# Optimization experiments

Measured on AMD Instinct MI355X. Metric: run time of the kernel, lower is better.

The kernel has to match this reference:

```python
import jax, jax.numpy as jnp
import numpy as np

D_MODEL, N_QUERY, N_HEAD = 1024, 2, 8
D_HEAD = D_MODEL // (N_QUERY * N_HEAD)  # 64
KV = D_HEAD * N_HEAD                    # 512


def setup_inputs() -> dict:
    key = jax.random.key(0)
    ks = jax.random.split(key, 6)
    B, S = 2, 2048
    x = jax.random.normal(ks[0], (B, S, D_MODEL), jnp.float32)
    Wq = jax.random.normal(ks[1], (D_MODEL, D_MODEL), jnp.float32) / np.sqrt(D_MODEL)
    Wk = jax.random.normal(ks[2], (D_MODEL, KV), jnp.float32) / np.sqrt(D_MODEL)
    Wv = jax.random.normal(ks[3], (D_MODEL, KV), jnp.float32) / np.sqrt(D_MODEL)
    memory = jax.random.normal(ks[4], (KV, KV), jnp.float32)
    memory_norm = jnp.ones((KV,), jnp.float32)
    memory_weight = jnp.ones((1,), jnp.float32)
    return {"x": x, "Wq": Wq, "Wk": Wk, "Wv": Wv,
            "memory": memory, "memory_norm": memory_norm,
            "memory_weight": memory_weight}


def reference(x, Wq, Wk, Wv, memory, memory_norm, memory_weight):
    B, S, _ = x.shape
    QH = N_QUERY * N_HEAD
    scale = 1.0 / jnp.sqrt(jnp.float32(D_HEAD))

    q = x @ Wq          # (B,S,D_MODEL)
    k = x @ Wk          # (B,S,KV)
    v = x @ Wv          # (B,S,KV)

    # --- Eq. 6: grouped scaled dot-product attention ---
    q4 = q.reshape(B, S, QH, D_HEAD)                    # flat query split
    k4 = jnp.repeat(k.reshape(B, S, N_HEAD, D_HEAD), N_QUERY, axis=2)  # (B,S,QH,D)
    v4 = jnp.repeat(v.reshape(B, S, N_HEAD, D_HEAD), N_QUERY, axis=2)
    scores = jnp.einsum('bsnd,btnd->bnst', q4, k4) * scale  # (B,QH,S,S)
    probs = jax.nn.softmax(scores, axis=-1)
    a_dot = jnp.einsum('bnst,btnd->bsnd', probs, v4)        # (B,S,QH,D)

    # --- Eq. 7: memory read (grouped over n_query, width n_head*d_head) ---
    sigma_q = jax.nn.elu(q.reshape(B, S, N_QUERY, KV))      # (B,S,Q,KV)
    num = sigma_q @ memory                                   # (B,S,Q,KV)
    den = (sigma_q @ memory_norm)[..., None]                 # (B,S,Q,1)
    a_mem = (num / den).reshape(B, S, QH, D_HEAD)

    # --- Eq. 8/9: memory update (delta rule) ---
    sigma_k = jax.nn.elu(k)                                  # (B,S,KV)
    retrieved = (sigma_k @ memory) / (sigma_k @ memory_norm)[..., None]
    new_memory = memory + jnp.einsum('bsk,bsv->kv', sigma_k, v - retrieved)
    new_memory_norm = memory_norm + jnp.sum(sigma_k, axis=(0, 1))

    # --- Eq. 10: sigmoid-gated fusion ---
    w = jax.nn.sigmoid(memory_weight)                        # (1,)
    out = (a_dot * (1.0 - w) + a_mem * w).reshape(B, S, D_MODEL)
    return out, new_memory, new_memory_norm
```

## Files before the change

### kernel.cpp

```cpp
#include <hip/hip_runtime.h>
#include <hip/hip_bf16.h>

#define BB 2
#define SS 2048
#define DM 1024
#define KVD 512
#define NH 8
#define NQ 2
#define QH 16
#define DH 64
#define MROWS 4096

typedef float f32x4 __attribute__((ext_vector_type(4)));
typedef short short8 __attribute__((ext_vector_type(8)));
typedef short short4v __attribute__((ext_vector_type(4)));
typedef unsigned uint2v __attribute__((ext_vector_type(2)));

__device__ __forceinline__ float elu_f(float x) {
    return x > 0.0f ? x : (__expf(x) - 1.0f);
}

__device__ __forceinline__ short f2bf(float f) {
    union { float f; unsigned u; } v; v.f = f;
    unsigned r = v.u + 0x7FFFu + ((v.u >> 16) & 1u);
    return (short)(r >> 16);
}
__device__ __forceinline__ float bf2f(short s) {
    union { unsigned u; float f; } v;
    v.u = ((unsigned)(unsigned short)s) << 16;
    return v.f;
}
__device__ __forceinline__ unsigned cvtpk(float lo, float hi) {
    unsigned u;
    asm("v_cvt_pk_bf16_f32 %0, %1, %2" : "=v"(u) : "v"(lo), "v"(hi));
    return u;
}

__device__ __forceinline__ int swzs(int row, int byteoff) {
    return (row * 128 + (byteoff ^ ((row & 7) << 4))) >> 1;
}

#define GLD16(gp, lp) __builtin_amdgcn_global_load_lds( \
    (const __attribute__((address_space(1))) void*)(gp), \
    (__attribute__((address_space(3))) void*)(lp), 16, 0, 0)

__device__ __forceinline__ void stage_gl(const short* __restrict__ src, int ld,
                                         int row0, int k0, short* L,
                                         int wv, int lane) {
    const int srow = lane >> 3, sslot = lane & 7;
    #pragma unroll
    for (int i = 0; i < 4; i++) {
        int row = wv * 32 + i * 8 + srow;
        int slot = sslot ^ (row & 7);
        GLD16(&src[(size_t)(row0 + row) * ld + k0 + slot * 8],
              &L[(wv * 32 + i * 8) * 64]);
    }
}

__device__ __forceinline__ void stage_gl64(const short* __restrict__ src, int ld,
                                           int row0, int k0, short* L,
                                           int wv, int lane) {
    const int srow = lane >> 3, sslot = lane & 7;
    #pragma unroll
    for (int i = 0; i < 2; i++) {
        int row = wv * 16 + i * 8 + srow;
        int slot = sslot ^ (row & 7);
        GLD16(&src[(size_t)(row0 + row) * ld + k0 + slot * 8],
              &L[(wv * 16 + i * 8) * 64]);
    }
}

__device__ __forceinline__ void mma_tile(const short* __restrict__ Als,
                                         const short* __restrict__ Bls,
                                         int mb, int nb, int qr, int kg,
                                         f32x4 acc[4][4]) {
    #pragma unroll
    for (int kc = 0; kc < 2; kc++) {
        short8 af[4], bg[4];
        #pragma unroll
        for (int mi = 0; mi < 4; mi++)
            af[mi] = *(const short8*)&Als[swzs(mb + mi * 16 + qr, kc * 64 + kg * 16)];
        #pragma unroll
        for (int ni = 0; ni < 4; ni++)
            bg[ni] = *(const short8*)&Bls[swzs(nb + ni * 16 + qr, kc * 64 + kg * 16)];
        #pragma unroll
        for (int mi = 0; mi < 4; mi++)
            #pragma unroll
            for (int ni = 0; ni < 4; ni++)
                acc[mi][ni] = __builtin_amdgcn_mfma_f32_16x16x32_bf16(
                    af[mi], bg[ni], acc[mi][ni], 0, 0, 0);
    }
}

__device__ __forceinline__ void mma_tile64(const short* __restrict__ Als,
                                           const short* __restrict__ Bls,
                                           int mb, int nb, int qr, int kg,
                                           f32x4 acc[2][2]) {
    #pragma unroll
    for (int kc = 0; kc < 2; kc++) {
        short8 af[2], bg[2];
        #pragma unroll
        for (int mi = 0; mi < 2; mi++)
            af[mi] = *(const short8*)&Als[swzs(mb + mi * 16 + qr, kc * 64 + kg * 16)];
        #pragma unroll
        for (int ni = 0; ni < 2; ni++)
            bg[ni] = *(const short8*)&Bls[swzs(nb + ni * 16 + qr, kc * 64 + kg * 16)];
        #pragma unroll
        for (int mi = 0; mi < 2; mi++)
            #pragma unroll
            for (int ni = 0; ni < 2; ni++)
                acc[mi][ni] = __builtin_amdgcn_mfma_f32_16x16x32_bf16(
                    af[mi], bg[ni], acc[mi][ni], 0, 0, 0);
    }
}

__global__ __launch_bounds__(256) void prep_all(
        const float* __restrict__ x, const float* __restrict__ Wq,
        const float* __restrict__ Wk, const float* __restrict__ Wv,
        const float* __restrict__ memory,
        short* __restrict__ xb, short* __restrict__ wtb,
        short* __restrict__ memtb, float* __restrict__ out_mem) {
    __shared__ float Ts[64][65];
    const int blk = blockIdx.x;
    const int tid = threadIdx.x;

    if (blk < 2048) {
        int i = (blk * 256 + tid) * 8;
        float4 a = *(const float4*)&x[i];
        float4 b = *(const float4*)&x[i + 4];
        short8 s;
        s[0] = f2bf(a.x); s[1] = f2bf(a.y); s[2] = f2bf(a.z); s[3] = f2bf(a.w);
        s[4] = f2bf(b.x); s[5] = f2bf(b.y); s[6] = f2bf(b.z); s[7] = f2bf(b.w);
        *(short8*)&xb[i] = s;
        return;
    }
    if (blk < 2560) {
        int idx = blk - 2048;
        const int k0 = (idx & 15) * 64, n0 = (idx >> 4) * 64;
        const float* W; int ld, c0;
        if (n0 < 1024)      { W = Wq; ld = 1024; c0 = n0; }
        else if (n0 < 1536) { W = Wk; ld = 512;  c0 = n0 - 1024; }
        else                { W = Wv; ld = 512;  c0 = n0 - 1536; }
        #pragma unroll
        for (int i = 0; i < 16; i++) {
            int e = tid + 256 * i;
            int kk = e >> 6, nn = e & 63;
            Ts[nn][kk] = W[(size_t)(k0 + kk) * ld + c0 + nn];
        }
        __syncthreads();
        #pragma unroll
        for (int i = 0; i < 16; i++) {
            int e = tid + 256 * i;
            int nn = e >> 6, kk = e & 63;
            wtb[(size_t)(n0 + nn) * 1024 + k0 + kk] = f2bf(Ts[nn][kk]);
        }
        return;
    }
    if (blk < 2624) {
        int idx = blk - 2560;
        const int k0 = (idx & 7) * 64, n0 = (idx >> 3) * 64;
        #pragma unroll
        for (int i = 0; i < 16; i++) {
            int e = tid + 256 * i;
            int kk = e >> 6, nn = e & 63;
            Ts[nn][kk] = memory[(size_t)(k0 + kk) * 512 + n0 + nn];
        }
        __syncthreads();
        #pragma unroll
        for (int i = 0; i < 16; i++) {
            int e = tid + 256 * i;
            int nn = e >> 6, kk = e & 63;
            memtb[(size_t)(n0 + nn) * 512 + k0 + kk] = f2bf(Ts[nn][kk]);
        }
        return;
    }
    {
        int idx = blk - 2624;
        int i = (idx * 256 + tid) * 4;
        *(float4*)&out_mem[i] = *(const float4*)&memory[i];
    }
}

__global__ __launch_bounds__(256) void gemm_qkv_mfma(
        const short* __restrict__ xb, const short* __restrict__ wtb,
        short* __restrict__ q, short* __restrict__ k, short* __restrict__ v,
        short* __restrict__ qelu, short* __restrict__ kelu,
        short* __restrict__ keluT, short* __restrict__ vt) {
    __shared__ __align__(16) short SMEM[32768];
    short (*Tls)[130] = (short(*)[130])SMEM;
    const int n0 = blockIdx.x * 128, m0 = blockIdx.y * 128;
    const int tid = threadIdx.x, lane = tid & 63, wv = tid >> 6;
    const int qr = lane & 15, kg = lane >> 4;
    const int mb = (wv >> 1) * 64, nb = (wv & 1) * 64;

    f32x4 acc[4][4];
    #pragma unroll
    for (int i = 0; i < 4; i++)
        #pragma unroll
        for (int j = 0; j < 4; j++) acc[i][j] = (f32x4){0.f, 0.f, 0.f, 0.f};

    stage_gl(xb, 1024, m0, 0, SMEM, wv, lane);
    stage_gl(wtb, 1024, n0, 0, SMEM + 8192, wv, lane);

    for (int kt = 0; kt < 16; kt++) {
        const int cur = kt & 1;
        short* Acur = SMEM + cur * 16384;
        short* Bcur = Acur + 8192;
        __syncthreads();
        if (kt + 1 < 16) {
            short* Anxt = SMEM + (cur ^ 1) * 16384;
            stage_gl(xb, 1024, m0, (kt + 1) * 64, Anxt, wv, lane);
            stage_gl(wtb, 1024, n0, (kt + 1) * 64, Anxt + 8192, wv, lane);
        }
        mma_tile(Acur, Bcur, mb, nb, qr, kg, acc);
    }
    __syncthreads();

    const int kind = (n0 < 1024) ? 0 : (n0 < 1536) ? 1 : 2;
    #pragma unroll
    for (int mi = 0; mi < 4; mi++)
        #pragma unroll
        for (int ni = 0; ni < 4; ni++)
            #pragma unroll
            for (int r = 0; r < 4; r++) {
                int lr = mb + mi * 16 + kg * 4 + r;
                int lc = nb + ni * 16 + qr;
                int gr = m0 + lr;
                short val = f2bf(acc[mi][ni][r]);
                if (kind == 0) {
                    int gc = n0 + lc;
                    q[(size_t)gr * 1024 + gc] = val;
                    qelu[(size_t)gr * 1024 + gc] = f2bf(elu_f(bf2f(val)));
                } else if (kind == 1) {
                    int gc = (n0 - 1024) + lc;
                    k[(size_t)gr * 512 + gc] = val;
                    short ev = f2bf(elu_f(bf2f(val)));
                    kelu[(size_t)gr * 512 + gc] = ev;
                    Tls[lr][lc] = ev;
                } else {
                    int gc = (n0 - 1536) + lc;
                    v[(size_t)gr * 512 + gc] = val;
                    Tls[lr][lc] = val;
                }
            }

    if (kind == 0) return;
    __syncthreads();
    const int lane16 = tid & 15, rgrp = tid >> 4;
    #pragma unroll
    for (int p = 0; p < 8; p++) {
        int lc2 = p * 16 + rgrp;
        short8 s;
        #pragma unroll
        for (int e = 0; e < 8; e++) s[e] = Tls[lane16 * 8 + e][lc2];
        if (kind == 1) {
            int gcT = (n0 - 1024) + lc2;
            *(short8*)&keluT[(size_t)gcT * 4096 + m0 + lane16 * 8] = s;
        } else {
            int gc = (n0 - 1536) + lc2;
            int bh2 = (m0 >> 11) * 8 + (gc >> 6);
            *(short8*)&vt[((size_t)bh2 * 64 + (gc & 63)) * SS + (m0 & 2047)
                          + lane16 * 8] = s;
        }
    }
}

__global__ __launch_bounds__(256) void den_colsum(
        const short* __restrict__ qelu, const short* __restrict__ kelu,
        const short* __restrict__ keluT, const float* __restrict__ norm,
        float* __restrict__ den_q, float* __restrict__ den_k,
        float* __restrict__ out_norm) {
    const int wavei = threadIdx.x >> 6, lane = threadIdx.x & 63;
    const int blk = blockIdx.x;
    if (blk < 3072) {
        const int row = blk * 4 + wavei;
        const short* src; float* den;
        if (row < 8192) { src = qelu + (size_t)row * 512; den = den_q + row; }
        else { int rk = row - 8192; src = kelu + (size_t)rk * 512; den = den_k + rk; }
        short8 vv = *(const short8*)&src[lane * 8];
        float4 n0 = *(const float4*)&norm[lane * 8];
        float4 n1 = *(const float4*)&norm[lane * 8 + 4];
        float nn[8] = {n0.x, n0.y, n0.z, n0.w, n1.x, n1.y, n1.z, n1.w};
        float s = 0.0f;
        #pragma unroll
        for (int j = 0; j < 8; j++) s += bf2f(vv[j]) * nn[j];
        #pragma unroll
        for (int off = 32; off >= 1; off >>= 1) s += __shfl_xor(s, off);
        if (lane == 0) *den = s;
    } else {
        const int row = (blk - 3072) * 4 + wavei;
        float s = 0.0f;
        #pragma unroll
        for (int j = 0; j < 8; j++) {
            short8 vv = *(const short8*)&keluT[(size_t)row * 4096 + j * 512 + lane * 8];
            #pragma unroll
            for (int e = 0; e < 8; e++) s += bf2f(vv[e]);
        }
        #pragma unroll
        for (int off = 32; off >= 1; off >>= 1) s += __shfl_xor(s, off);
        if (lane == 0) out_norm[row] = norm[row] + s;
    }
}

__global__ __launch_bounds__(256) void gemm_amem_mfma(
        const short* __restrict__ qelu, const short* __restrict__ memtb,
        const short* __restrict__ adotb, const float* __restrict__ den_q,
        const float* __restrict__ mw, float* __restrict__ out) {
    __shared__ __align__(16) short SMEM[16384];
    const int n0 = blockIdx.x * 64, m0 = blockIdx.y * 64;
    const int tid = threadIdx.x, lane = tid & 63, wv = tid >> 6;
    const int qr = lane & 15, kg = lane >> 4;
    const int mb = (wv >> 1) * 32, nb = (wv & 1) * 32;
    const float wgt = 1.0f / (1.0f + __expf(-mw[0]));

    f32x4 acc[2][2];
    #pragma unroll
    for (int i = 0; i < 2; i++)
        #pragma unroll
        for (int j = 0; j < 2; j++) acc[i][j] = (f32x4){0.f, 0.f, 0.f, 0.f};

    stage_gl64(qelu, 512, m0, 0, SMEM, wv, lane);
    stage_gl64(memtb, 512, n0, 0, SMEM + 4096, wv, lane);
    for (int kt = 0; kt < 8; kt++) {
        const int cur = kt & 1;
        short* Acur = SMEM + cur * 8192;
        short* Bcur = Acur + 4096;
        __syncthreads();
        if (kt + 1 < 8) {
            short* Anxt = SMEM + (cur ^ 1) * 8192;
            stage_gl64(qelu, 512, m0, (kt + 1) * 64, Anxt, wv, lane);
            stage_gl64(memtb, 512, n0, (kt + 1) * 64, Anxt + 4096, wv, lane);
        }
        mma_tile64(Acur, Bcur, mb, nb, qr, kg, acc);
    }

    #pragma unroll
    for (int mi = 0; mi < 2; mi++) {
        int gr0 = m0 + mb + mi * 16 + kg * 4;
        float invd[4];
        #pragma unroll
        for (int r = 0; r < 4; r++) invd[r] = wgt / den_q[gr0 + r];
        #pragma unroll
        for (int ni = 0; ni < 2; ni++) {
            int gc = n0 + nb + ni * 16 + qr;
            #pragma unroll
            for (int r = 0; r < 4; r++) {
                size_t fo = (size_t)(gr0 + r) * 512 + gc;
                out[fo] = bf2f(adotb[fo]) * (1.0f - wgt)
                        + acc[mi][ni][r] * invd[r];
            }
        }
    }
}

__global__ __launch_bounds__(256) void gemm_u_mfma(
        const short* __restrict__ kelu, const short* __restrict__ memtb,
        const short* __restrict__ vb, const float* __restrict__ den_k,
        short* __restrict__ uT) {
    __shared__ __align__(16) short SMEM[16384];
    const int n0 = blockIdx.x * 64, m0 = blockIdx.y * 64;
    const int tid = threadIdx.x, lane = tid & 63, wv = tid >> 6;
    const int qr = lane & 15, kg = lane >> 4;
    const int mb = (wv >> 1) * 32, nb = (wv & 1) * 32;

    f32x4 acc[2][2];
    #pragma unroll
    for (int i = 0; i < 2; i++)
        #pragma unroll
        for (int j = 0; j < 2; j++) acc[i][j] = (f32x4){0.f, 0.f, 0.f, 0.f};

    stage_gl64(kelu, 512, m0, 0, SMEM, wv, lane);
    stage_gl64(memtb, 512, n0, 0, SMEM + 4096, wv, lane);
    for (int kt = 0; kt < 8; kt++) {
        const int cur = kt & 1;
        short* Acur = SMEM + cur * 8192;
        short* Bcur = Acur + 4096;
        __syncthreads();
        if (kt + 1 < 8) {
            short* Anxt = SMEM + (cur ^ 1) * 8192;
            stage_gl64(kelu, 512, m0, (kt + 1) * 64, Anxt, wv, lane);
            stage_gl64(memtb, 512, n0, (kt + 1) * 64, Anxt + 4096, wv, lane);
        }
        mma_tile64(Acur, Bcur, mb, nb, qr, kg, acc);
    }

    #pragma unroll
    for (int mi = 0; mi < 2; mi++) {
        int gr0 = m0 + mb + mi * 16 + kg * 4;
        float invd[4];
        #pragma unroll
        for (int r = 0; r < 4; r++) invd[r] = 1.0f / den_k[gr0 + r];
        #pragma unroll
        for (int ni = 0; ni < 2; ni++) {
            int gc = n0 + nb + ni * 16 + qr;
            short4v st;
            #pragma unroll
            for (int r = 0; r < 4; r++)
                st[r] = f2bf(bf2f(vb[(size_t)(gr0 + r) * 512 + gc])
                             - acc[mi][ni][r] * invd[r]);
            *(short4v*)&uT[(size_t)gc * 4096 + gr0] = st;
        }
    }
}

__global__ __launch_bounds__(256) void gemm_delta_mfma(
        const short* __restrict__ keluT, const short* __restrict__ uT,
        float* __restrict__ out_mem) {
    __shared__ __align__(16) short SMEM[16384];
    const int j0 = blockIdx.x * 64, i0 = blockIdx.y * 64;
    const int kcz = blockIdx.z;
    const int tid = threadIdx.x, lane = tid & 63, wv = tid >> 6;
    const int qr = lane & 15, kg = lane >> 4;
    const int mb = (wv >> 1) * 32, nb = (wv & 1) * 32;

    f32x4 acc[2][2];
    #pragma unroll
    for (int i = 0; i < 2; i++)
        #pragma unroll
        for (int j = 0; j < 2; j++) acc[i][j] = (f32x4){0.f, 0.f, 0.f, 0.f};

    stage_gl64(keluT, 4096, i0, kcz * 512, SMEM, wv, lane);
    stage_gl64(uT, 4096, j0, kcz * 512, SMEM + 4096, wv, lane);
    for (int kt = 0; kt < 8; kt++) {
        const int cur = kt & 1;
        short* Acur = SMEM + cur * 8192;
        short* Bcur = Acur + 4096;
        __syncthreads();
        if (kt + 1 < 8) {
            int k0 = kcz * 512 + (kt + 1) * 64;
            short* Anxt = SMEM + (cur ^ 1) * 8192;
            stage_gl64(keluT, 4096, i0, k0, Anxt, wv, lane);
            stage_gl64(uT, 4096, j0, k0, Anxt + 4096, wv, lane);
        }
        mma_tile64(Acur, Bcur, mb, nb, qr, kg, acc);
    }

    #pragma unroll
    for (int mi = 0; mi < 2; mi++)
        #pragma unroll
        for (int ni = 0; ni < 2; ni++)
            #pragma unroll
            for (int r = 0; r < 4; r++) {
                int gr = i0 + mb + mi * 16 + kg * 4 + r;
                int gc = j0 + nb + ni * 16 + qr;
                atomicAdd(&out_mem[(size_t)gr * 512 + gc], acc[mi][ni][r]);
            }
}

__global__ __launch_bounds__(256) void flash_attn_mfma(
        const short* __restrict__ qb, const short* __restrict__ kb,
        const short* __restrict__ vt, short* __restrict__ adotb) {
    __shared__ __align__(16) short Klds[2][4096];
    __shared__ __align__(16) short Vlds[2][4096];
    __shared__ __align__(16) short Plds[4096];

    const int id = blockIdx.x;
    const int low3 = id & 7, rest = id >> 3;
    const int xblk = rest & 31, bhhi = rest >> 5;
    const int bh = (bhhi << 3) | low3;
    const int r0 = xblk * 64;
    const int b = bh >> 4, qh = bh & 15;
    const int kvh = qh >> 1;
    const int tid = threadIdx.x;
    const int lane = tid & 63, wv = tid >> 6;
    const int qr = lane & 15, kg = lane >> 4;
    const float scale2 = 0.125f * 1.44269504f;

    const int srow = lane >> 3, sslot = lane & 7;

    const int krow0 = wv * 16 + srow, krow1 = krow0 + 8;
    const short* kp0 = kb + (size_t)(b * SS + krow0) * KVD + kvh * DH
                       + (sslot ^ (krow0 & 7)) * 8;
    const short* kp1 = kb + (size_t)(b * SS + krow1) * KVD + kvh * DH
                       + (sslot ^ (krow1 & 7)) * 8;
    const short* vp0 = vt + ((size_t)(b * NH + kvh) * DH + krow0) * SS
                       + (sslot ^ (krow0 & 7)) * 8;
    const short* vp1 = vt + ((size_t)(b * NH + kvh) * DH + krow1) * SS
                       + (sslot ^ (krow1 & 7)) * 8;

    short8 qa[2];
    {
        const short* qp = qb + (size_t)(b * SS + r0 + wv * 16 + qr) * DM + qh * DH;
        qa[0] = *(const short8*)&qp[kg * 8];
        qa[1] = *(const short8*)&qp[32 + kg * 8];
        #pragma unroll
        for (int e = 0; e < 8; e++) {
            qa[0][e] = f2bf(bf2f(qa[0][e]) * scale2);
            qa[1][e] = f2bf(bf2f(qa[1][e]) * scale2);
        }
    }
    short8 ones;
    #pragma unroll
    for (int e = 0; e < 8; e++) ones[e] = (short)0x3F80;

    f32x4 oacc[4];
    #pragma unroll
    for (int dt = 0; dt < 4; dt++) oacc[dt] = (f32x4){0.f, 0.f, 0.f, 0.f};
    f32x4 lacc = (f32x4){0.f, 0.f, 0.f, 0.f};

    short* Pw = Plds + wv * 1024;
    short* Kdst0 = &Klds[0][(wv * 16 + 0) * 64];
    short* Kdst1 = &Klds[0][(wv * 16 + 8) * 64];
    short* Vdst0 = &Vlds[0][(wv * 16 + 0) * 64];
    short* Vdst1 = &Vlds[0][(wv * 16 + 8) * 64];

    GLD16(kp0, Kdst0); GLD16(kp1, Kdst1);
    GLD16(vp0, Vdst0); GLD16(vp1, Vdst1);

    for (int it = 0; it < 32; ++it) {
        const int cur = it & 1;
        __syncthreads();
        if (it + 1 < 32) {
            kp0 += 64 * KVD; kp1 += 64 * KVD; vp0 += 64; vp1 += 64;
            int nb2 = (cur ^ 1) * 4096;
            GLD16(kp0, Kdst0 + nb2); GLD16(kp1, Kdst1 + nb2);
            GLD16(vp0, Vdst0 + nb2); GLD16(vp1, Vdst1 + nb2);
        }

        f32x4 sacc[4];
        #pragma unroll
        for (int j = 0; j < 4; j++) sacc[j] = (f32x4){0.f, 0.f, 0.f, 0.f};
        __builtin_amdgcn_s_setprio(1);
        #pragma unroll
        for (int c = 0; c < 2; c++) {
            #pragma unroll
            for (int j = 0; j < 4; j++) {
                short8 kf = *(const short8*)&Klds[cur][swzs(j * 16 + qr, kg * 16 + c * 64)];
                sacc[j] = __builtin_amdgcn_mfma_f32_16x16x32_bf16(kf, qa[c], sacc[j], 0, 0, 0);
            }
        }
        __builtin_amdgcn_s_setprio(0);

        #pragma unroll
        for (int j = 0; j < 4; j++) {
            float p0 = exp2f(sacc[j][0]);
            float p1 = exp2f(sacc[j][1]);
            float p2 = exp2f(sacc[j][2]);
            float p3 = exp2f(sacc[j][3]);
            uint2v u;
            u[0] = cvtpk(p0, p1);
            u[1] = cvtpk(p2, p3);
            *(uint2v*)&Pw[swzs(qr, j * 32 + kg * 8)] = u;
        }
        asm volatile("s_waitcnt lgkmcnt(0)" ::: "memory");
        __builtin_amdgcn_sched_barrier(0);

        __builtin_amdgcn_s_setprio(1);
        #pragma unroll
        for (int c = 0; c < 2; c++) {
            short8 pf = *(const short8*)&Pw[swzs(qr, kg * 16 + c * 64)];
            lacc = __builtin_amdgcn_mfma_f32_16x16x32_bf16(ones, pf, lacc, 0, 0, 0);
            #pragma unroll
            for (int dt = 0; dt < 4; dt++) {
                short8 vf = *(const short8*)&Vlds[cur][swzs(dt * 16 + qr, kg * 16 + c * 64)];
                oacc[dt] = __builtin_amdgcn_mfma_f32_16x16x32_bf16(vf, pf, oacc[dt], 0, 0, 0);
            }
        }
        __builtin_amdgcn_s_setprio(0);
    }

    float inv = 1.0f / lacc[0];
    short* ap = adotb + (size_t)(b * SS + r0 + wv * 16 + qr) * DM + qh * DH;
    #pragma unroll
    for (int dt = 0; dt < 4; dt++) {
        short4v st;
        #pragma unroll
        for (int r = 0; r < 4; r++) st[r] = f2bf(oacc[dt][r] * inv);
        *(short4v*)&ap[dt * 16 + kg * 4] = st;
    }
}

extern "C" void kernel_launch(void* const* d_in, const int* in_sizes, int n_in,
                              void* d_out, int out_size, void* d_ws, size_t ws_size,
                              hipStream_t stream) {
    const float* x      = (const float*)d_in[0];
    const float* Wq     = (const float*)d_in[1];
    const float* Wk     = (const float*)d_in[2];
    const float* Wv     = (const float*)d_in[3];
    const float* memory = (const float*)d_in[4];
    const float* mnorm  = (const float*)d_in[5];
    const float* mw     = (const float*)d_in[6];

    float* out_f   = (float*)d_out;
    float* out_mem = out_f + (size_t)MROWS * DM;
    float* out_nrm = out_mem + (size_t)KVD * KVD;

    short*  xb    = (short*)d_ws;
    short*  wtb   = xb + 4194304;
    short*  memtb = wtb + 2097152;
    short*  qb    = memtb + 262144;
    short*  kbuf  = qb + 4194304;
    short*  vbuf  = kbuf + 2097152;
    short*  vt    = vbuf + 2097152;
    short*  qelu  = vt + 2097152;
    short*  kelu  = qelu + 4194304;
    short*  keluT = kelu + 2097152;
    short*  uT    = keluT + 2097152;
    float*  den_q = (float*)(uT + 2097152);
    float*  den_k = den_q + 8192;
    short*  adotb = xb;

    prep_all<<<2880, 256, 0, stream>>>(x, Wq, Wk, Wv, memory, xb, wtb, memtb,
                                       out_mem);

    gemm_qkv_mfma<<<dim3(16, 32), 256, 0, stream>>>(xb, wtb, qb, kbuf, vbuf,
                                                    qelu, kelu, keluT, vt);

    flash_attn_mfma<<<1024, 256, 0, stream>>>(qb, kbuf, vt, adotb);

    den_colsum<<<3200, 256, 0, stream>>>(qelu, kelu, keluT, mnorm,
                                         den_q, den_k, out_nrm);

    gemm_amem_mfma<<<dim3(8, 128), 256, 0, stream>>>(qelu, memtb, adotb,
                                                     den_q, mw, out_f);

    gemm_u_mfma<<<dim3(8, 64), 256, 0, stream>>>(kelu, memtb, vbuf, den_k, uT);
    gemm_delta_mfma<<<dim3(8, 8, 8), 256, 0, stream>>>(keluT, uT, out_mem);
}
```

Baseline: 147.3 us.

## Split attention KV tile across wave pairs with 512-thread blocks and LDS reduction

Doubles the flash-attention block to 8 waves, pairing waves so each handles half of every 64-key tile for the same 16 query rows. Each wave computes half the scores, writes a smaller P tile, and accumulates partial O and row sums, which are combined through LDS at the end. The aim is more waves in flight to hide latency in the per-tile compute chain. In exchange it adds a final reduction with extra syncs, duplicates the Q loads, and shrinks the MFMA work per wave.

Result: slower. 152.8 us (+3.7%).

```diff
diff --git a/kernel.cpp b/kernel.cpp
--- a/kernel.cpp
+++ b/kernel.cpp
@@ -38,6 +38,9 @@
 
 __device__ __forceinline__ int swzs(int row, int byteoff) {
     return (row * 128 + (byteoff ^ ((row & 7) << 4))) >> 1;
+}
+__device__ __forceinline__ int swz32(int row, int byteoff) {
+    return (row * 64 + (byteoff ^ ((row & 3) << 4))) >> 1;
 }
 
 #define GLD16(gp, lp) __builtin_amdgcn_global_load_lds( \
@@ -447,7 +450,7 @@
             }
 }
 
-__global__ __launch_bounds__(256) void flash_attn_mfma(
+__global__ __launch_bounds__(512) void flash_attn_mfma(
         const short* __restrict__ qb, const short* __restrict__ kb,
         const short* __restrict__ vt, short* __restrict__ adotb) {
     __shared__ __align__(16) short Klds[2][4096];
@@ -463,24 +466,21 @@
     const int kvh = qh >> 1;
     const int tid = threadIdx.x;
     const int lane = tid & 63, wv = tid >> 6;
+    const int pair = wv >> 1, half = wv & 1;
     const int qr = lane & 15, kg = lane >> 4;
     const float scale2 = 0.125f * 1.44269504f;
 
     const int srow = lane >> 3, sslot = lane & 7;
 
-    const int krow0 = wv * 16 + srow, krow1 = krow0 + 8;
-    const short* kp0 = kb + (size_t)(b * SS + krow0) * KVD + kvh * DH
-                       + (sslot ^ (krow0 & 7)) * 8;
-    const short* kp1 = kb + (size_t)(b * SS + krow1) * KVD + kvh * DH
-                       + (sslot ^ (krow1 & 7)) * 8;
-    const short* vp0 = vt + ((size_t)(b * NH + kvh) * DH + krow0) * SS
-                       + (sslot ^ (krow0 & 7)) * 8;
-    const short* vp1 = vt + ((size_t)(b * NH + kvh) * DH + krow1) * SS
-                       + (sslot ^ (krow1 & 7)) * 8;
+    const int krow = wv * 8 + srow;
+    const short* kp = kb + (size_t)(b * SS + krow) * KVD + kvh * DH
+                      + (sslot ^ (krow & 7)) * 8;
+    const short* vp = vt + ((size_t)(b * NH + kvh) * DH + krow) * SS
+                      + (sslot ^ (krow & 7)) * 8;
 
     short8 qa[2];
     {
-        const short* qp = qb + (size_t)(b * SS + r0 + wv * 16 + qr) * DM + qh * DH;
+        const short* qp = qb + (size_t)(b * SS + r0 + pair * 16 + qr) * DM + qh * DH;
         qa[0] = *(const short8*)&qp[kg * 8];
         qa[1] = *(const short8*)&qp[32 + kg * 8];
         #pragma unroll
@@ -498,75 +498,89 @@
     for (int dt = 0; dt < 4; dt++) oacc[dt] = (f32x4){0.f, 0.f, 0.f, 0.f};
     f32x4 lacc = (f32x4){0.f, 0.f, 0.f, 0.f};
 
-    short* Pw = Plds + wv * 1024;
-    short* Kdst0 = &Klds[0][(wv * 16 + 0) * 64];
-    short* Kdst1 = &Klds[0][(wv * 16 + 8) * 64];
-    short* Vdst0 = &Vlds[0][(wv * 16 + 0) * 64];
-    short* Vdst1 = &Vlds[0][(wv * 16 + 8) * 64];
-
-    GLD16(kp0, Kdst0); GLD16(kp1, Kdst1);
-    GLD16(vp0, Vdst0); GLD16(vp1, Vdst1);
+    short* Pw = Plds + wv * 512;
+    short* Kdst = &Klds[0][wv * 512];
+    short* Vdst = &Vlds[0][wv * 512];
+
+    GLD16(kp, Kdst);
+    GLD16(vp, Vdst);
 
     for (int it = 0; it < 32; ++it) {
         const int cur = it & 1;
         __syncthreads();
         if (it + 1 < 32) {
-            kp0 += 64 * KVD; kp1 += 64 * KVD; vp0 += 64; vp1 += 64;
+            kp += 64 * KVD; vp += 64;
             int nb2 = (cur ^ 1) * 4096;
-            GLD16(kp0, Kdst0 + nb2); GLD16(kp1, Kdst1 + nb2);
-            GLD16(vp0, Vdst0 + nb2); GLD16(vp1, Vdst1 + nb2);
-        }
-
-        f32x4 sacc[4];
-        #pragma unroll
-        for (int j = 0; j < 4; j++) sacc[j] = (f32x4){0.f, 0.f, 0.f, 0.f};
+            GLD16(kp, Kdst + nb2);
+            GLD16(vp, Vdst + nb2);
+        }
+
+        f32x4 sacc[2];
+        sacc[0] = (f32x4){0.f, 0.f, 0.f, 0.f};
+        sacc[1] = (f32x4){0.f, 0.f, 0.f, 0.f};
         __builtin_amdgcn_s_setprio(1);
         #pragma unroll
         for (int c = 0; c < 2; c++) {
             #pragma unroll
-            for (int j = 0; j < 4; j++) {
+            for (int jj = 0; jj < 2; jj++) {
+                int j = half * 2 + jj;
                 short8 kf = *(const short8*)&Klds[cur][swzs(j * 16 + qr, kg * 16 + c * 64)];
-                sacc[j] = __builtin_amdgcn_mfma_f32_16x16x32_bf16(kf, qa[c], sacc[j], 0, 0, 0);
+                sacc[jj] = __builtin_amdgcn_mfma_f32_16x16x32_bf16(kf, qa[c], sacc[jj], 0, 0, 0);
             }
         }
         __builtin_amdgcn_s_setprio(0);
 
         #pragma unroll
-        for (int j = 0; j < 4; j++) {
-            float p0 = exp2f(sacc[j][0]);
-            float p1 = exp2f(sacc[j][1]);
-            float p2 = exp2f(sacc[j][2]);
-            float p3 = exp2f(sacc[j][3]);
+        for (int jj = 0; jj < 2; jj++) {
+            float p0 = exp2f(sacc[jj][0]);
+            float p1 = exp2f(sacc[jj][1]);
+            float p2 = exp2f(sacc[jj][2]);
+            float p3 = exp2f(sacc[jj][3]);
             uint2v u;
             u[0] = cvtpk(p0, p1);
             u[1] = cvtpk(p2, p3);
-            *(uint2v*)&Pw[swzs(qr, j * 32 + kg * 8)] = u;
+            *(uint2v*)&Pw[swz32(qr, jj * 32 + kg * 8)] = u;
         }
         asm volatile("s_waitcnt lgkmcnt(0)" ::: "memory");
         __builtin_amdgcn_sched_barrier(0);
 
         __builtin_amdgcn_s_setprio(1);
-        #pragma unroll
-        for (int c = 0; c < 2; c++) {
-            short8 pf = *(const short8*)&Pw[swzs(qr, kg * 16 + c * 64)];
+        {
+            short8 pf = *(const short8*)&Pw[swz32(qr, kg * 16)];
             lacc = __builtin_amdgcn_mfma_f32_16x16x32_bf16(ones, pf, lacc, 0, 0, 0);
             #pragma unroll
             for (int dt = 0; dt < 4; dt++) {
-                short8 vf = *(const short8*)&Vlds[cur][swzs(dt * 16 + qr, kg * 16 + c * 64)];
+                short8 vf = *(const short8*)&Vlds[cur][swzs(dt * 16 + qr,
+                                                           kg * 16 + half * 64)];
                 oacc[dt] = __builtin_amdgcn_mfma_f32_16x16x32_bf16(vf, pf, oacc[dt], 0, 0, 0);
             }
         }
         __builtin_amdgcn_s_setprio(0);
     }
 
-    float inv = 1.0f / lacc[0];
-    short* ap = adotb + (size_t)(b * SS + r0 + wv * 16 + qr) * DM + qh * DH;
-    #pragma unroll
-    for (int dt = 0; dt < 4; dt++) {
-        short4v st;
-        #pragma unroll
-        for (int r = 0; r < 4; r++) st[r] = f2bf(oacc[dt][r] * inv);
-        *(short4v*)&ap[dt * 16 + kg * 4] = st;
+    __syncthreads();
+    float* Ored = (float*)&Klds[0][0];
+    const int slot = (pair * 64 + lane) * 17;
+    if (half == 1) {
+        #pragma unroll
+        for (int dt = 0; dt < 4; dt++)
+            #pragma unroll
+            for (int r = 0; r < 4; r++) Ored[slot + dt * 4 + r] = oacc[dt][r];
+        Ored[slot + 16] = lacc[0];
+    }
+    __syncthreads();
+    if (half == 0) {
+        float l = lacc[0] + Ored[slot + 16];
+        float inv = 1.0f / l;
+        short* ap = adotb + (size_t)(b * SS + r0 + pair * 16 + qr) * DM + qh * DH;
+        #pragma unroll
+        for (int dt = 0; dt < 4; dt++) {
+            short4v st;
+            #pragma unroll
+            for (int r = 0; r < 4; r++)
+                st[r] = f2bf((oacc[dt][r] + Ored[slot + dt * 4 + r]) * inv);
+            *(short4v*)&ap[dt * 16 + kg * 4] = st;
+        }
     }
 }
 
@@ -606,7 +620,7 @@
     gemm_qkv_mfma<<<dim3(16, 32), 256, 0, stream>>>(xb, wtb, qb, kbuf, vbuf,
                                                     qelu, kelu, keluT, vt);
 
-    flash_attn_mfma<<<1024, 256, 0, stream>>>(qb, kbuf, vt, adotb);
+    flash_attn_mfma<<<1024, 512, 0, stream>>>(qb, kbuf, vt, adotb);
 
     den_colsum<<<3200, 256, 0, stream>>>(qelu, kelu, keluT, mnorm,
                                          den_q, den_k, out_nrm);
```
